# Optimization experiments

Measured on AMD Instinct MI355X. Metric: run time of the kernel, lower is better.

Reference implementation:

```python
import jax, jax.numpy as jnp
import numpy as np

N = 100_000        # nodes
E = 1_600_000      # edges
G = 256            # graphs in batch
C_IN = 128
NUM_CLASSES = 10


def _rn(k, shape, s=0.1):
    return jax.random.normal(k, shape, jnp.float32) * s


def setup_inputs() -> dict:
    key = jax.random.key(0)
    ks = jax.random.split(key, 32)
    inp = {
        "x": jax.random.normal(ks[0], (N, C_IN), jnp.float32),
        "edge_index": jax.random.randint(ks[1], (2, E), 0, N, jnp.int64) if jax.config.jax_enable_x64 else jax.random.randint(ks[1], (2, E), 0, N, jnp.int32),
        "batch": jnp.sort(jax.random.randint(ks[2], (N,), 0, G)),
        "tolerance": jax.random.normal(ks[3], (1, 1), jnp.float32),
        "cost": jax.random.normal(ks[4], (1, 1), jnp.float32),
        "time": jax.random.normal(ks[5], (1, 1), jnp.float32),
        "quantity": jax.random.normal(ks[6], (1, 1), jnp.float32),
        # GCNConv weights (x @ W then aggregate, + bias)
        "W1": _rn(ks[7], (C_IN, 64)), "b1": _rn(ks[8], (64,)),
        "W2": _rn(ks[9], (64, 16)), "b2": _rn(ks[10], (16,)),
        # residual projections
        "Wr1": _rn(ks[11], (C_IN, 64)), "br1": _rn(ks[12], (64,)),
        "Wr2": _rn(ks[13], (64, 16)), "br2": _rn(ks[14], (16,)),
        "alpha1": jnp.float32(0.5), "alpha2": jnp.float32(0.5),
        # 4 metrics MLPs stacked: Linear(1,8) -> SiLU -> Linear(8,16)
        "mW1": _rn(ks[15], (4, 1, 8)), "mb1": _rn(ks[16], (4, 8)),
        "mW2": _rn(ks[17], (4, 8, 16)), "mb2": _rn(ks[18], (4, 16)),
        # classifier head
        "Wf1": _rn(ks[19], (80, 80)), "bf1": _rn(ks[20], (80,)),
        "Wf2": _rn(ks[21], (80, NUM_CLASSES)), "bf2": _rn(ks[22], (NUM_CLASSES,)),
    }
    return inp


def _gcn_norm(src, dst, n):
    # add self loops, symmetric normalization: norm_e = d^-1/2[src] * d^-1/2[dst]
    loop = jnp.arange(n, dtype=src.dtype)
    src2 = jnp.concatenate([src, loop])
    dst2 = jnp.concatenate([dst, loop])
    deg = jax.ops.segment_sum(jnp.ones_like(dst2, jnp.float32), dst2, num_segments=n)
    dinv = jnp.where(deg > 0, jax.lax.rsqrt(jnp.maximum(deg, 1.0)), 0.0)
    norm = dinv[src2] * dinv[dst2]
    return src2, dst2, norm


def _gcn_conv(x, W, b, src2, dst2, norm, n):
    h = x @ W                                 # [N, out]
    msg = h[src2] * norm[:, None]             # gather + scale  [E+N, out]
    return jax.ops.segment_sum(msg, dst2, num_segments=n) + b


def reference(x, edge_index, batch, tolerance, cost, time, quantity,
              W1, b1, W2, b2, Wr1, br1, Wr2, br2, alpha1, alpha2,
              mW1, mb1, mW2, mb2, Wf1, bf1, Wf2, bf2):
    silu = jax.nn.silu
    n = x.shape[0]
    src2, dst2, norm = _gcn_norm(edge_index[0], edge_index[1], n)

    # encoder
    r1 = silu(x @ Wr1 + br1)
    h = silu(_gcn_conv(x, W1, b1, src2, dst2, norm, n))
    h = h + r1 * alpha1
    r2 = silu(h @ Wr2 + br2)
    z = _gcn_conv(h, W2, b2, src2, dst2, norm, n)
    z = z + r2 * alpha2                       # [N, 16]

    # global mean pool over graphs
    sums = jax.ops.segment_sum(z, batch, num_segments=G)
    cnts = jax.ops.segment_sum(jnp.ones((n,), z.dtype), batch, num_segments=G)
    graph_emb = sums / jnp.maximum(cnts, 1.0)[:, None]   # [G, 16]

    # metrics embedding: 4 tiny MLPs, stacked  m:[4,1,1]
    m = jnp.stack([tolerance, cost, time, quantity])
    e = silu(jnp.einsum('gij,gjk->gik', m, mW1) + mb1[:, None, :])
    e = jnp.einsum('gij,gjk->gik', e, mW2) + mb2[:, None, :]   # [4,1,16]
    metrics = jnp.tile(e.transpose(1, 0, 2).reshape(1, 64), (G, 1))  # [G,64]

    combined = jnp.concatenate([graph_emb, metrics], axis=1)  # [G, 80]
    out = silu(combined @ Wf1 + bf1)
    return out @ Wf2 + bf2                                    # [G, num_classes]
```

## Files before the change

### kernel.cpp

```cpp
#include <hip/hip_runtime.h>

static __device__ __forceinline__ float silu_f(float v) {
    return v / (1.0f + __expf(-v));
}


extern "C" __global__ __launch_bounds__(256) void k_bhist(
    const int* __restrict__ dst, int* __restrict__ bcount, int E, int nbkt, int shift)
{
    __shared__ int lh[512];
    int t = threadIdx.x;
    for (int i = t; i < 512; i += 256) lh[i] = 0;
    __syncthreads();
    int e0 = blockIdx.x * 8192;
    #pragma unroll 4
    for (int i = 0; i < 32; i++) {
        int e = e0 + t + i * 256;
        if (e < E) atomicAdd(&lh[dst[e] >> shift], 1);
    }
    __syncthreads();
    for (int b = t; b < nbkt; b += 256)
        if (lh[b]) atomicAdd(&bcount[b], lh[b]);
}

extern "C" __global__ __launch_bounds__(512) void k_bscan(
    const int* __restrict__ bcount, int* __restrict__ boff, int* __restrict__ bcursor, int nbkt)
{
    __shared__ int sc[512];
    int t = threadIdx.x;
    int v = (t < nbkt) ? bcount[t] : 0;
    sc[t] = v;
    __syncthreads();
    for (int off = 1; off < 512; off <<= 1) {
        int add = (t >= off) ? sc[t - off] : 0;
        __syncthreads();
        sc[t] += add;
        __syncthreads();
    }
    int excl = sc[t] - v;
    if (t < nbkt) { boff[t] = excl; bcursor[t] = excl; }
    if (t == nbkt - 1) boff[nbkt] = excl + v;
}

extern "C" __global__ __launch_bounds__(256) void k_bscatter(
    const int* __restrict__ src, const int* __restrict__ dst, int* __restrict__ bcursor,
    int2* __restrict__ ebuf, int E, int nbkt, int shift)
{
    __shared__ int lh[512];
    __shared__ int lbase[512];
    int t = threadIdx.x;
    for (int i = t; i < 512; i += 256) lh[i] = 0;
    __syncthreads();
    int e0 = blockIdx.x * 8192;
    #pragma unroll 4
    for (int i = 0; i < 32; i++) {
        int e = e0 + t + i * 256;
        if (e < E) atomicAdd(&lh[dst[e] >> shift], 1);
    }
    __syncthreads();
    for (int b = t; b < nbkt; b += 256)
        lbase[b] = lh[b] ? atomicAdd(&bcursor[b], lh[b]) : 0;
    __syncthreads();
    #pragma unroll 4
    for (int i = 0; i < 32; i++) {
        int e = e0 + t + i * 256;
        if (e < E) {
            int d = dst[e];
            int p = atomicAdd(&lbase[d >> shift], 1);
            ebuf[p] = make_int2(src[e], d);
        }
    }
}

extern "C" __global__ __launch_bounds__(256) void k_bdeg_scan(
    const int2* __restrict__ ebuf, const int* __restrict__ boff,
    int* __restrict__ deg, float* __restrict__ dinv, int* __restrict__ rowstart,
    int shift, int N)
{
    int b = blockIdx.x;
    int W = 1 << shift;
    __shared__ int lcur[4096];
    __shared__ int sc[256];
    int t = threadIdx.x;
    for (int i = t; i < W; i += 256) lcur[i] = 0;
    __syncthreads();
    int s = boff[b], e_ = boff[b + 1];
    for (int e = s + t; e < e_; e += 256)
        atomicAdd(&lcur[ebuf[e].y - (b << shift)], 1);
    __syncthreads();

    int c = W >> 8;
    int base = t * c;
    int mysum = 0;
    for (int i = 0; i < c; i++) mysum += lcur[base + i];
    sc[t] = mysum;
    __syncthreads();
    int mine = mysum;
    for (int off = 1; off < 256; off <<= 1) {
        int add = (t >= off) ? sc[t - off] : 0;
        __syncthreads();
        sc[t] += add;
        __syncthreads();
    }
    int run = sc[t] - mine + s;
    int nbase = b << shift;
    for (int i = 0; i < c; i++) {
        int d = lcur[base + i];
        int node = nbase + base + i;
        if (node < N) {
            rowstart[node] = run;
            deg[node] = d;
            dinv[node] = rsqrtf((float)(d + 1));
        }
        run += d;
    }
}

extern "C" __global__ __launch_bounds__(256) void k_bfill(
    const int2* __restrict__ ebuf, const int* __restrict__ boff,
    const int* __restrict__ rowstart, int* __restrict__ csr, int shift)
{
    int b = blockIdx.x;
    int W = 1 << shift;
    __shared__ int lcur[4096];
    int t = threadIdx.x;
    for (int i = t; i < W; i += 256) lcur[i] = 0;
    __syncthreads();
    int s = boff[b], e_ = boff[b + 1];
    for (int e = s + t; e < e_; e += 256) {
        int2 p = ebuf[e];
        int pos = atomicAdd(&lcur[p.y - (b << shift)], 1);
        csr[rowstart[p.y] + pos] = p.x;
    }
}

extern "C" __global__ __launch_bounds__(256) void k_gemm1(
    const float* __restrict__ x, const float* __restrict__ W1, const float* __restrict__ Wr1,
    const float* __restrict__ br1, const float* __restrict__ dinv,
    float* __restrict__ h0s, float* __restrict__ r1, int n)
{
    __shared__ float xs[128 * 33];
    int t = threadIdx.x;
    int lane = t & 63;
    int wv = __builtin_amdgcn_readfirstlane(t >> 6);
    const float* Wp = (wv < 2) ? W1 : Wr1;
    const int c0 = (wv & 1) * 32;
    int r0 = blockIdx.x * 128;

    float acc0[32] = {}, acc1[32] = {};

    for (int kk = 0; kk < 128; kk += 32) {
        if (kk) __syncthreads();
        #pragma unroll
        for (int i = 0; i < 4; i++) {
            int u = t + i * 256;
            int rr = u >> 3, kq = u & 7;
            float4 v = make_float4(0.f, 0.f, 0.f, 0.f);
            if (r0 + rr < n) v = *(const float4*)&x[(size_t)(r0 + rr) * 128 + kk + kq * 4];
            xs[rr * 33 + kq * 4 + 0] = v.x;
            xs[rr * 33 + kq * 4 + 1] = v.y;
            xs[rr * 33 + kq * 4 + 2] = v.z;
            xs[rr * 33 + kq * 4 + 3] = v.w;
        }
        __syncthreads();
        const float* xr0 = &xs[lane * 33];
        const float* xr1 = &xs[(lane + 64) * 33];
        #pragma unroll 4
        for (int k = 0; k < 32; k++) {
            float xv0 = xr0[k];
            float xv1 = xr1[k];
            const float* wrow = &Wp[(size_t)(kk + k) * 64 + c0];
            #pragma unroll
            for (int j = 0; j < 8; j++) {
                float4 w4 = *(const float4*)&wrow[j * 4];
                acc0[j*4+0] += xv0 * w4.x; acc1[j*4+0] += xv1 * w4.x;
                acc0[j*4+1] += xv0 * w4.y; acc1[j*4+1] += xv1 * w4.y;
                acc0[j*4+2] += xv0 * w4.z; acc1[j*4+2] += xv1 * w4.z;
                acc0[j*4+3] += xv0 * w4.w; acc1[j*4+3] += xv1 * w4.w;
            }
        }
    }

    #pragma unroll
    for (int half = 0; half < 2; half++) {
        int row = r0 + half * 64 + lane;
        if (row >= n) continue;
        const float* a = half ? acc1 : acc0;
        if (wv < 2) {
            float dv = dinv[row];
            #pragma unroll
            for (int j = 0; j < 8; j++) {
                float4 o = make_float4(a[j*4+0]*dv, a[j*4+1]*dv, a[j*4+2]*dv, a[j*4+3]*dv);
                *(float4*)&h0s[(size_t)row * 64 + c0 + j * 4] = o;
            }
        } else {
            #pragma unroll
            for (int j = 0; j < 8; j++) {
                float4 b = *(const float4*)&br1[c0 + j * 4];
                float4 o = make_float4(silu_f(a[j*4+0]+b.x), silu_f(a[j*4+1]+b.y),
                                       silu_f(a[j*4+2]+b.z), silu_f(a[j*4+3]+b.w));
                *(float4*)&r1[(size_t)row * 64 + c0 + j * 4] = o;
            }
        }
    }
}

extern "C" __global__ __launch_bounds__(256) void k_agg1(
    const float* __restrict__ h0s, const int* __restrict__ rowstart, const int* __restrict__ deg,
    const int* __restrict__ csr, const float* __restrict__ dinv, const float* __restrict__ b1,
    const float* __restrict__ alpha1, float* __restrict__ r1h, int n)
{
    int wave = threadIdx.x >> 6, lane = threadIdx.x & 63;
    int node = blockIdx.x * 4 + wave;
    if (node >= n) return;
    int rs = rowstart[node];
    int cnt = deg[node];
    float acc = h0s[(size_t)node * 64 + lane];
    int i = 0;
    for (; i + 8 <= cnt; i += 8) {
        int s0 = csr[rs+i+0], s1 = csr[rs+i+1], s2 = csr[rs+i+2], s3 = csr[rs+i+3];
        int s4 = csr[rs+i+4], s5 = csr[rs+i+5], s6 = csr[rs+i+6], s7 = csr[rs+i+7];
        float a0 = h0s[(size_t)s0*64+lane], a1 = h0s[(size_t)s1*64+lane];
        float a2 = h0s[(size_t)s2*64+lane], a3 = h0s[(size_t)s3*64+lane];
        float a4 = h0s[(size_t)s4*64+lane], a5 = h0s[(size_t)s5*64+lane];
        float a6 = h0s[(size_t)s6*64+lane], a7 = h0s[(size_t)s7*64+lane];
        acc += ((a0+a1)+(a2+a3)) + ((a4+a5)+(a6+a7));
    }
    for (; i < cnt; i++) acc += h0s[(size_t)csr[rs+i]*64+lane];
    float v = dinv[node] * acc + b1[lane];
    float hv = silu_f(v) + r1h[(size_t)node * 64 + lane] * alpha1[0];
    r1h[(size_t)node * 64 + lane] = hv;
}

extern "C" __global__ __launch_bounds__(256) void k_gemm2(
    const float* __restrict__ h, const float* __restrict__ W2, const float* __restrict__ Wr2,
    const float* __restrict__ br2, const float* __restrict__ dinv,
    float* __restrict__ h2s, float* __restrict__ r2, int n)
{
    __shared__ float xsT[64 * 132];
    __shared__ float wsm[64 * 32];
    int t = threadIdx.x;
    int r0 = blockIdx.x * 128;
    int rg = t >> 3;
    int cg = t & 7;
    float acc[4][4] = {};

    #pragma unroll
    for (int i = 0; i < 8; i++) {
        int u = t + i * 256;
        int row = u >> 4, kq = u & 15;
        float4 v = make_float4(0.f, 0.f, 0.f, 0.f);
        int grow = r0 + row;
        if (grow < n) v = *(const float4*)&h[(size_t)grow * 64 + kq * 4];
        xsT[(kq * 4 + 0) * 132 + row] = v.x;
        xsT[(kq * 4 + 1) * 132 + row] = v.y;
        xsT[(kq * 4 + 2) * 132 + row] = v.z;
        xsT[(kq * 4 + 3) * 132 + row] = v.w;
    }
    #pragma unroll
    for (int i = 0; i < 2; i++) {
        int ul = t + i * 256;
        int k = ul >> 3, u = ul & 7;
        int c = u * 4;
        float4 v;
        if (c < 16) v = *(const float4*)&W2[(size_t)k * 16 + c];
        else        v = *(const float4*)&Wr2[(size_t)k * 16 + (c - 16)];
        *(float4*)&wsm[k * 32 + c] = v;
    }
    __syncthreads();

    const float* xbase = &xsT[rg * 4];
    const float* wbase = &wsm[cg * 4];
    #pragma unroll
    for (int k = 0; k < 64; k++) {
        float4 xa = *(const float4*)&xbase[k * 132];
        float4 wa = *(const float4*)&wbase[k * 32];
        float xv[4] = {xa.x, xa.y, xa.z, xa.w};
        float wv[4] = {wa.x, wa.y, wa.z, wa.w};
        #pragma unroll
        for (int i = 0; i < 4; i++)
            #pragma unroll
            for (int j = 0; j < 4; j++) acc[i][j] += xv[i] * wv[j];
    }

    if (cg < 4) {
        int c0 = cg * 4;
        #pragma unroll
        for (int i = 0; i < 4; i++) {
            int row = r0 + rg * 4 + i;
            if (row >= n) break;
            float dv = dinv[row];
            float4 o = make_float4(acc[i][0]*dv, acc[i][1]*dv, acc[i][2]*dv, acc[i][3]*dv);
            *(float4*)&h2s[(size_t)row * 16 + c0] = o;
        }
    } else {
        int c0 = (cg - 4) * 4;
        float4 b = *(const float4*)&br2[c0];
        #pragma unroll
        for (int i = 0; i < 4; i++) {
            int row = r0 + rg * 4 + i;
            if (row >= n) break;
            float4 o = make_float4(silu_f(acc[i][0]+b.x), silu_f(acc[i][1]+b.y),
                                   silu_f(acc[i][2]+b.z), silu_f(acc[i][3]+b.w));
            *(float4*)&r2[(size_t)row * 16 + c0] = o;
        }
    }
}

extern "C" __global__ __launch_bounds__(256) void k_agg2(
    const float* __restrict__ h2s, const int* __restrict__ rowstart, const int* __restrict__ deg,
    const int* __restrict__ csr, const float* __restrict__ dinv, const float* __restrict__ b2,
    const float* __restrict__ alpha2, float* __restrict__ r2z, int n)
{
    int wave = threadIdx.x >> 6, lane = threadIdx.x & 63;
    int node = blockIdx.x * 4 + wave;
    if (node >= n) return;
    int rs = rowstart[node], cnt = deg[node];
    int sub = lane >> 4, j = lane & 15;
    float acc = 0.0f;
    int i = sub;
    for (; i + 8 <= cnt; i += 8) {
        int sa = csr[rs + i], sb = csr[rs + i + 4];
        acc += h2s[(size_t)sa * 16 + j] + h2s[(size_t)sb * 16 + j];
    }
    for (; i < cnt; i += 4) acc += h2s[(size_t)csr[rs + i] * 16 + j];
    acc += __shfl_xor(acc, 16, 64);
    acc += __shfl_xor(acc, 32, 64);
    if (sub == 0) {
        acc += h2s[(size_t)node * 16 + j];
        float v = dinv[node] * acc + b2[j] + r2z[(size_t)node * 16 + j] * alpha2[0];
        r2z[(size_t)node * 16 + j] = v;
    }
}

extern "C" __global__ __launch_bounds__(256) void k_poolhead(
    const float* __restrict__ z, const int* __restrict__ batch,
    const float* __restrict__ tol, const float* __restrict__ cost,
    const float* __restrict__ time_, const float* __restrict__ qty,
    const float* __restrict__ mW1, const float* __restrict__ mb1,
    const float* __restrict__ mW2, const float* __restrict__ mb2,
    const float* __restrict__ Wf1, const float* __restrict__ bf1,
    const float* __restrict__ Wf2, const float* __restrict__ bf2,
    float* __restrict__ out, int n, int NC)
{
    int g = blockIdx.x;
    __shared__ float comb[80];
    __shared__ float part[16][17];
    __shared__ float hidden[80];
    int t = threadIdx.x;

    int lo = 0, hi = n;
    while (lo < hi) { int m = (lo + hi) >> 1; if (batch[m] < g) lo = m + 1; else hi = m; }
    int start = lo;
    lo = start; hi = n;
    while (lo < hi) { int m = (lo + hi) >> 1; if (batch[m] < g + 1) lo = m + 1; else hi = m; }
    int end = lo;

    int j = t & 15, grp = t >> 4;
    float acc = 0.0f;
    for (int r = start + grp; r < end; r += 16) acc += z[(size_t)r * 16 + j];
    part[grp][j] = acc;
    __syncthreads();
    if (t < 16) {
        float s = 0.0f;
        #pragma unroll
        for (int q = 0; q < 16; q++) s += part[q][t];
        comb[t] = s / fmaxf((float)(end - start), 1.0f);
    } else if (t >= 64 && t < 128) {
        int tt = t - 64;
        int i = tt >> 4, jj = tt & 15;
        float mv = (i == 0) ? tol[0] : (i == 1) ? cost[0] : (i == 2) ? time_[0] : qty[0];
        float a = mb2[i * 16 + jj];
        #pragma unroll
        for (int k = 0; k < 8; k++) {
            float hpre = mv * mW1[i * 8 + k] + mb1[i * 8 + k];
            a += silu_f(hpre) * mW2[i * 128 + k * 16 + jj];
        }
        comb[16 + tt] = a;
    }
    __syncthreads();
    if (t < 80) {
        float a = bf1[t];
        #pragma unroll 8
        for (int k = 0; k < 80; k++) a += comb[k] * Wf1[k * 80 + t];
        hidden[t] = silu_f(a);
    }
    __syncthreads();
    if (t < NC) {
        float a = bf2[t];
        #pragma unroll 8
        for (int k = 0; k < 80; k++) a += hidden[k] * Wf2[k * NC + t];
        out[g * NC + t] = a;
    }
}

extern "C" void kernel_launch(void* const* d_in, const int* in_sizes, int n_in,
                              void* d_out, int out_size, void* d_ws, size_t ws_size,
                              hipStream_t stream)
{
    const float* x     = (const float*)d_in[0];
    const int*   ei    = (const int*)d_in[1];
    const int*   batch = (const int*)d_in[2];
    const float* tol   = (const float*)d_in[3];
    const float* cost  = (const float*)d_in[4];
    const float* time_ = (const float*)d_in[5];
    const float* qty   = (const float*)d_in[6];
    const float* W1    = (const float*)d_in[7];
    const float* b1    = (const float*)d_in[8];
    const float* W2    = (const float*)d_in[9];
    const float* b2    = (const float*)d_in[10];
    const float* Wr1   = (const float*)d_in[11];
    const float* br1   = (const float*)d_in[12];
    const float* Wr2   = (const float*)d_in[13];
    const float* br2   = (const float*)d_in[14];
    const float* alpha1= (const float*)d_in[15];
    const float* alpha2= (const float*)d_in[16];
    const float* mW1   = (const float*)d_in[17];
    const float* mb1   = (const float*)d_in[18];
    const float* mW2   = (const float*)d_in[19];
    const float* mb2   = (const float*)d_in[20];
    const float* Wf1   = (const float*)d_in[21];
    const float* bf1   = (const float*)d_in[22];
    const float* Wf2   = (const float*)d_in[23];
    const float* bf2   = (const float*)d_in[24];

    const int N  = in_sizes[2];
    const int E  = in_sizes[1] / 2;
    const int NC = in_sizes[24];
    const int G  = out_size / NC;

    const int* srcIdx = ei;
    const int* dstIdx = ei + E;

    int shift = 8;
    while (((N + (1 << shift) - 1) >> shift) > 512) shift++;
    const int nbkt = (N + (1 << shift) - 1) >> shift;

    char* w = (char*)d_ws;
    auto alloc = [&](size_t bytes) { char* p = w; w += (bytes + 255) & ~(size_t)255; return p; };
    int*   deg      = (int*)alloc((size_t)N * 4);
    int*   rowstart = (int*)alloc((size_t)N * 4);
    int*   bcount   = (int*)alloc(2048);
    int*   boff     = (int*)alloc(2052 + 252);
    int*   bcursor  = (int*)alloc(2048);
    int*   csr      = (int*)alloc((size_t)E * 4);
    int2*  ebuf     = (int2*)alloc((size_t)E * 8);
    float* dinv     = (float*)alloc((size_t)N * 4);
    float* bufA     = (float*)alloc((size_t)N * 64 * 4);
    float* bufB     = (float*)alloc((size_t)N * 64 * 4);
    float* bufC     = (float*)alloc((size_t)N * 16 * 4);

    hipMemsetAsync(bcount, 0, 2048, stream);

    int EB8 = (E + 8191) / 8192;

    k_bhist    <<<EB8, 256, 0, stream>>>(dstIdx, bcount, E, nbkt, shift);
    k_bscan    <<<1, 512, 0, stream>>>(bcount, boff, bcursor, nbkt);
    k_bscatter <<<EB8, 256, 0, stream>>>(srcIdx, dstIdx, bcursor, ebuf, E, nbkt, shift);
    k_bdeg_scan<<<nbkt, 256, 0, stream>>>(ebuf, boff, deg, dinv, rowstart, shift, N);
    k_bfill    <<<nbkt, 256, 0, stream>>>(ebuf, boff, rowstart, csr, shift);

    k_gemm1<<<(N + 127) / 128, 256, 0, stream>>>(x, W1, Wr1, br1, dinv, bufA, bufB, N);
    k_agg1 <<<(N + 3) / 4, 256, 0, stream>>>(bufA, rowstart, deg, csr, dinv, b1, alpha1, bufB, N);
    k_gemm2<<<(N + 127) / 128, 256, 0, stream>>>(bufB, W2, Wr2, br2, dinv, bufA, bufC, N);
    k_agg2 <<<(N + 3) / 4, 256, 0, stream>>>(bufA, rowstart, deg, csr, dinv, b2, alpha2, bufC, N);
    k_poolhead<<<G, 256, 0, stream>>>(bufC, batch, tol, cost, time_, qty,
                                      mW1, mb1, mW2, mb2, Wf1, bf1, Wf2, bf2,
                                      (float*)d_out, N, NC);
}
```

Baseline: 289.5 us.

## Widen gemm1 to 512 threads with register prefetch and split agg1 features across blocks

k_gemm1 now runs 8 waves per block, each computing 16 output columns instead of 32. It prefetches the next x tile into registers while computing the current one and uses padded float4 LDS stores and reads. k_agg1 is restructured so each block handles an 8-feature slice of 4 nodes: the 8 lanes of a group read contiguous features and 8 groups stride over neighbours, then combine with shuffles. This aims to raise memory-level parallelism and occupancy, but the aggregation launches 8x more blocks and reads each CSR index list 8 times, and the gather uses only 32-byte segments.

```diff
diff --git a/kernel.cpp b/kernel.cpp
--- a/kernel.cpp
+++ b/kernel.cpp
@@ -134,49 +134,66 @@
     }
 }
 
-extern "C" __global__ __launch_bounds__(256) void k_gemm1(
+extern "C" __global__ __launch_bounds__(512) void k_gemm1(
     const float* __restrict__ x, const float* __restrict__ W1, const float* __restrict__ Wr1,
     const float* __restrict__ br1, const float* __restrict__ dinv,
     float* __restrict__ h0s, float* __restrict__ r1, int n)
 {
-    __shared__ float xs[128 * 33];
+    __shared__ float xs[128 * 36];
     int t = threadIdx.x;
     int lane = t & 63;
     int wv = __builtin_amdgcn_readfirstlane(t >> 6);
-    const float* Wp = (wv < 2) ? W1 : Wr1;
-    const int c0 = (wv & 1) * 32;
+    const float* Wp = (wv < 4) ? W1 : Wr1;
+    const int c0 = (wv & 3) * 16;
     int r0 = blockIdx.x * 128;
 
-    float acc0[32] = {}, acc1[32] = {};
+    float acc0[16] = {}, acc1[16] = {};
+    float4 px[2];
+
+    #pragma unroll
+    for (int i = 0; i < 2; i++) {
+        int u = t + i * 512;
+        int rr = u >> 3, kq = u & 7;
+        px[i] = make_float4(0.f, 0.f, 0.f, 0.f);
+        if (r0 + rr < n) px[i] = *(const float4*)&x[(size_t)(r0 + rr) * 128 + kq * 4];
+    }
 
     for (int kk = 0; kk < 128; kk += 32) {
         if (kk) __syncthreads();
         #pragma unroll
-        for (int i = 0; i < 4; i++) {
-            int u = t + i * 256;
+        for (int i = 0; i < 2; i++) {
+            int u = t + i * 512;
             int rr = u >> 3, kq = u & 7;
-            float4 v = make_float4(0.f, 0.f, 0.f, 0.f);
-            if (r0 + rr < n) v = *(const float4*)&x[(size_t)(r0 + rr) * 128 + kk + kq * 4];
-            xs[rr * 33 + kq * 4 + 0] = v.x;
-            xs[rr * 33 + kq * 4 + 1] = v.y;
-            xs[rr * 33 + kq * 4 + 2] = v.z;
-            xs[rr * 33 + kq * 4 + 3] = v.w;
+            *(float4*)&xs[rr * 36 + kq * 4] = px[i];
         }
         __syncthreads();
-        const float* xr0 = &xs[lane * 33];
-        const float* xr1 = &xs[(lane + 64) * 33];
-        #pragma unroll 4
-        for (int k = 0; k < 32; k++) {
-            float xv0 = xr0[k];
-            float xv1 = xr1[k];
-            const float* wrow = &Wp[(size_t)(kk + k) * 64 + c0];
+        if (kk < 96) {
+            int kn = kk + 32;
             #pragma unroll
-            for (int j = 0; j < 8; j++) {
-                float4 w4 = *(const float4*)&wrow[j * 4];
-                acc0[j*4+0] += xv0 * w4.x; acc1[j*4+0] += xv1 * w4.x;
-                acc0[j*4+1] += xv0 * w4.y; acc1[j*4+1] += xv1 * w4.y;
-                acc0[j*4+2] += xv0 * w4.z; acc1[j*4+2] += xv1 * w4.z;
-                acc0[j*4+3] += xv0 * w4.w; acc1[j*4+3] += xv1 * w4.w;
+            for (int i = 0; i < 2; i++) {
+                int u = t + i * 512;
+                int rr = u >> 3, kq = u & 7;
+                px[i] = make_float4(0.f, 0.f, 0.f, 0.f);
+                if (r0 + rr < n) px[i] = *(const float4*)&x[(size_t)(r0 + rr) * 128 + kn + kq * 4];
+            }
+        }
+        #pragma unroll
+        for (int kb = 0; kb < 8; kb++) {
+            float4 xa = *(const float4*)&xs[lane * 36 + kb * 4];
+            float4 xb = *(const float4*)&xs[(lane + 64) * 36 + kb * 4];
+            float xv0[4] = {xa.x, xa.y, xa.z, xa.w};
+            float xv1[4] = {xb.x, xb.y, xb.z, xb.w};
+            #pragma unroll
+            for (int kq = 0; kq < 4; kq++) {
+                const float* wrow = &Wp[(size_t)(kk + kb * 4 + kq) * 64 + c0];
+                #pragma unroll
+                for (int j = 0; j < 4; j++) {
+                    float4 w4 = *(const float4*)&wrow[j * 4];
+                    acc0[j*4+0] += xv0[kq] * w4.x; acc1[j*4+0] += xv1[kq] * w4.x;
+                    acc0[j*4+1] += xv0[kq] * w4.y; acc1[j*4+1] += xv1[kq] * w4.y;
+                    acc0[j*4+2] += xv0[kq] * w4.z; acc1[j*4+2] += xv1[kq] * w4.z;
+                    acc0[j*4+3] += xv0[kq] * w4.w; acc1[j*4+3] += xv1[kq] * w4.w;
+                }
             }
         }
     }
@@ -186,16 +203,16 @@
         int row = r0 + half * 64 + lane;
         if (row >= n) continue;
         const float* a = half ? acc1 : acc0;
-        if (wv < 2) {
+        if (wv < 4) {
             float dv = dinv[row];
             #pragma unroll
-            for (int j = 0; j < 8; j++) {
+            for (int j = 0; j < 4; j++) {
                 float4 o = make_float4(a[j*4+0]*dv, a[j*4+1]*dv, a[j*4+2]*dv, a[j*4+3]*dv);
                 *(float4*)&h0s[(size_t)row * 64 + c0 + j * 4] = o;
             }
         } else {
             #pragma unroll
-            for (int j = 0; j < 8; j++) {
+            for (int j = 0; j < 4; j++) {
                 float4 b = *(const float4*)&br1[c0 + j * 4];
                 float4 o = make_float4(silu_f(a[j*4+0]+b.x), silu_f(a[j*4+1]+b.y),
                                        silu_f(a[j*4+2]+b.z), silu_f(a[j*4+3]+b.w));
@@ -210,26 +227,31 @@
     const int* __restrict__ csr, const float* __restrict__ dinv, const float* __restrict__ b1,
     const float* __restrict__ alpha1, float* __restrict__ r1h, int n)
 {
-    int wave = threadIdx.x >> 6, lane = threadIdx.x & 63;
-    int node = blockIdx.x * 4 + wave;
+    int t = threadIdx.x;
+    int wave = t >> 6, lane = t & 63;
+    int s = blockIdx.x & 7;
+    int node = (blockIdx.x >> 3) * 4 + wave;
     if (node >= n) return;
-    int rs = rowstart[node];
-    int cnt = deg[node];
-    float acc = h0s[(size_t)node * 64 + lane];
-    int i = 0;
-    for (; i + 8 <= cnt; i += 8) {
-        int s0 = csr[rs+i+0], s1 = csr[rs+i+1], s2 = csr[rs+i+2], s3 = csr[rs+i+3];
-        int s4 = csr[rs+i+4], s5 = csr[rs+i+5], s6 = csr[rs+i+6], s7 = csr[rs+i+7];
-        float a0 = h0s[(size_t)s0*64+lane], a1 = h0s[(size_t)s1*64+lane];
-        float a2 = h0s[(size_t)s2*64+lane], a3 = h0s[(size_t)s3*64+lane];
-        float a4 = h0s[(size_t)s4*64+lane], a5 = h0s[(size_t)s5*64+lane];
-        float a6 = h0s[(size_t)s6*64+lane], a7 = h0s[(size_t)s7*64+lane];
-        acc += ((a0+a1)+(a2+a3)) + ((a4+a5)+(a6+a7));
-    }
-    for (; i < cnt; i++) acc += h0s[(size_t)csr[rs+i]*64+lane];
-    float v = dinv[node] * acc + b1[lane];
-    float hv = silu_f(v) + r1h[(size_t)node * 64 + lane] * alpha1[0];
-    r1h[(size_t)node * 64 + lane] = hv;
+    int f = lane & 7;
+    int sub = lane >> 3;
+    int fc = s * 8 + f;
+    int rs = rowstart[node], cnt = deg[node];
+    float acc = 0.0f;
+    int i = sub;
+    for (; i + 16 <= cnt; i += 16) {
+        int sa = csr[rs + i], sb = csr[rs + i + 8];
+        acc += h0s[(size_t)sa * 64 + fc] + h0s[(size_t)sb * 64 + fc];
+    }
+    for (; i < cnt; i += 8) acc += h0s[(size_t)csr[rs + i] * 64 + fc];
+    acc += __shfl_xor(acc, 8, 64);
+    acc += __shfl_xor(acc, 16, 64);
+    acc += __shfl_xor(acc, 32, 64);
+    if (sub == 0) {
+        acc += h0s[(size_t)node * 64 + fc];
+        float v = dinv[node] * acc + b1[fc];
+        float hv = silu_f(v) + r1h[(size_t)node * 64 + fc] * alpha1[0];
+        r1h[(size_t)node * 64 + fc] = hv;
+    }
 }
 
 extern "C" __global__ __launch_bounds__(256) void k_gemm2(
@@ -460,8 +482,8 @@
     k_bdeg_scan<<<nbkt, 256, 0, stream>>>(ebuf, boff, deg, dinv, rowstart, shift, N);
     k_bfill    <<<nbkt, 256, 0, stream>>>(ebuf, boff, rowstart, csr, shift);
 
-    k_gemm1<<<(N + 127) / 128, 256, 0, stream>>>(x, W1, Wr1, br1, dinv, bufA, bufB, N);
-    k_agg1 <<<(N + 3) / 4, 256, 0, stream>>>(bufA, rowstart, deg, csr, dinv, b1, alpha1, bufB, N);
+    k_gemm1<<<(N + 127) / 128, 512, 0, stream>>>(x, W1, Wr1, br1, dinv, bufA, bufB, N);
+    k_agg1 <<<8 * ((N + 3) / 4), 256, 0, stream>>>(bufA, rowstart, deg, csr, dinv, b1, alpha1, bufB, N);
     k_gemm2<<<(N + 127) / 128, 256, 0, stream>>>(bufB, W2, Wr2, br2, dinv, bufA, bufC, N);
     k_agg2 <<<(N + 3) / 4, 256, 0, stream>>>(bufA, rowstart, deg, csr, dinv, b2, alpha2, bufC, N);
     k_poolhead<<<G, 256, 0, stream>>>(bufC, batch, tol, cost, time_, qty,
```

Result: slower. 509.2 us (+75.9%).
